# Optimization experiments

Hardware: AMD Instinct MI355X
Metric: run time of the kernel (lower is better)

## Reference

```python
import jax, jax.numpy as jnp
import numpy as np

EPS = 1e-8       # epsilon added to abs-diff in compute_sim
LN_EPS = 1e-5    # torch nn.LayerNorm default eps
NUM_HEADS = 8


def _layernorm(x, g, b):
    mu = jnp.mean(x, axis=-1, keepdims=True)
    var = jnp.mean((x - mu) ** 2, axis=-1, keepdims=True)
    return (x - mu) / jnp.sqrt(var + LN_EPS) * g + b


def _fla(x, alphas, betas):
    # x: [B, D]; alphas/betas: [H, 3] scalars per (head, {query,key,value})
    D = x.shape[-1]
    scale = 1.0 / jnp.sqrt(jnp.float32(D))
    acc = jnp.zeros_like(x)
    for h in range(alphas.shape[0]):  # small fixed head count; avoids H*B*D*D blowup
        q = alphas[h, 0] * x + betas[h, 0]
        k = alphas[h, 1] * x + betas[h, 1]
        v = alphas[h, 2] * x + betas[h, 2]
        # sim[b,i,j] = 1/(|q[b,j]-k[b,i]|+eps), softmax over j, scaled by 1/sqrt(D)
        sim = jax.nn.softmax(1.0 / (jnp.abs(q[:, None, :] - k[:, :, None]) + EPS), axis=-1) * scale
        acc = acc + jnp.einsum('bij,bj->bi', sim, v)
    return x + acc


def setup_inputs() -> dict:
    key = jax.random.key(0)
    ks = jax.random.split(key, 8)
    B, D, L = 1024, 256, 2  # batch, feature dim (input_dim == hidden dims), num hidden layers
    x = jax.random.normal(ks[0], (B, D), dtype=jnp.float32)
    fla_alphas = jax.random.uniform(ks[1], (L, NUM_HEADS, 3), dtype=jnp.float32)
    fla_betas = jax.random.uniform(ks[2], (L, NUM_HEADS, 3), dtype=jnp.float32)
    lim = 1.0 / np.sqrt(D)
    lin_W = jax.random.uniform(ks[3], (L, D, D), dtype=jnp.float32, minval=-lim, maxval=lim)
    lin_b = jax.random.uniform(ks[4], (L, D), dtype=jnp.float32, minval=-lim, maxval=lim)
    fla_ln_g = jnp.ones((L, D), jnp.float32)
    fla_ln_b = jnp.zeros((L, D), jnp.float32)
    lin_ln_g = jnp.ones((L, D), jnp.float32)
    lin_ln_b = jnp.zeros((L, D), jnp.float32)
    out_W = jax.random.uniform(ks[5], (D, 1), dtype=jnp.float32, minval=-lim, maxval=lim)
    out_b = jax.random.uniform(ks[6], (1,), dtype=jnp.float32, minval=-lim, maxval=lim)
    return dict(x=x, fla_alphas=fla_alphas, fla_betas=fla_betas,
                fla_ln_g=fla_ln_g, fla_ln_b=fla_ln_b,
                lin_W=lin_W, lin_b=lin_b,
                lin_ln_g=lin_ln_g, lin_ln_b=lin_ln_b,
                out_W=out_W, out_b=out_b)


def reference(x, fla_alphas, fla_betas, fla_ln_g, fla_ln_b,
              lin_W, lin_b, lin_ln_g, lin_ln_b, out_W, out_b):
    L = fla_alphas.shape[0]
    for i in range(L):
        x = _fla(x, fla_alphas[i], fla_betas[i])
        x = jax.nn.relu(x)
        x = _layernorm(x, fla_ln_g[i], fla_ln_b[i])
        x = x @ lin_W[i] + lin_b[i]
        x = jax.nn.relu(x)
        x = _layernorm(x, lin_ln_g[i], lin_ln_b[i])
    return x @ out_W + out_b
```

## Files before the change

### kernel.cpp

```cpp
#include <hip/hip_runtime.h>

#define DD 256
#define NH 8
#define HPT 2
#define NHG 4

constexpr float LN_EPS = 1e-5f;
constexpr float SCALE  = 0.0625f;
constexpr float KS     = 8.2629579e-8f;
constexpr float B_EXP  = 1064986816.0f;
constexpr float T0     = 1.36150e8f;
#define RCP_MAGIC 0x7EF311C3u

__device__ __forceinline__ float wexp_clamped(float dh, float Bh) {
    float y = __uint_as_float(RCP_MAGIC - __float_as_uint(dh));
    float w = fmaf(-fabsf(dh), fabsf(y), 2.0f);
    float f = fminf(fmaf(fabsf(y), w, Bh), B_EXP);
    unsigned u;
    asm("v_cvt_u32_f32 %0, %1" : "=v"(u) : "v"(f));
    return __uint_as_float(u);
}

__device__ __forceinline__ int lb256(const float* __restrict__ a, float t) {
    int p = 0;
    #pragma unroll
    for (int st = 128; st > 0; st >>= 1)
        p += (a[p + st - 1] < t) ? st : 0;
    return p;
}

__device__ __forceinline__ unsigned f2s(float f) {
    unsigned u = __float_as_uint(f);
    return (u & 0x80000000u) ? ~u : (u | 0x80000000u);
}
__device__ __forceinline__ float s2f(unsigned s) {
    unsigned u = (s & 0x80000000u) ? (s ^ 0x80000000u) : ~s;
    return __uint_as_float(u);
}

__device__ __forceinline__ float2 fla_head(const float* __restrict__ xsrt,
                                           float aqk, float ck) {
    float inv_aqk = __builtin_amdgcn_rcpf(aqk);
    float xstar = fminf(fmaxf(-ck * inv_aqk, -1e5f), 1e5f);
    int pos = lb256(xsrt, xstar);
    pos += (xsrt[pos] < xstar) ? 1 : 0;
    int i1 = (pos - 1 > 0) ? pos - 1 : 0;
    int i2 = (pos < DD - 1) ? pos : DD - 1;
    float x2 = xsrt[i2];
    float d1 = fabsf(fmaf(aqk, xsrt[i1], ck));
    float d2 = fabsf(fmaf(aqk, x2, ck));
    float dm = fminf(d1, d2);
    float ym = __uint_as_float(RCP_MAGIC - __float_as_uint(dm));
    float m  = fabsf(ym) * fmaf(-dm, fabsf(ym), 2.0f);
    float Bh = B_EXP - m;
    float mm = fmaf(m, 0.9375f, -T0);
    float halfw = (mm > 0.f) ? __builtin_amdgcn_rcpf(mm) * fabsf(inv_aqk)
                             : 3e38f;
    float vlo = xstar - halfw;
    float vhi = fmaxf(xstar + halfw, x2);
    int lo = lb256(xsrt, vlo); lo = (lo < i1) ? lo : i1;
    int hi = lb256(xsrt, vhi); hi += (xsrt[hi] < vhi) ? 1 : 0;
    hi = (hi > i2 + 1) ? hi : i2 + 1;

    const float4* xs4 = reinterpret_cast<const float4*>(xsrt);
    const int cLo = lo >> 2, cHi = (hi - 1) >> 2;
    float sE0=0.f,sE1=0.f,sE2=0.f,sE3=0.f;
    float sW0=0.f,sW1=0.f,sW2=0.f,sW3=0.f;
    #pragma unroll 2
    for (int ci = cLo; ci <= cHi; ++ci) {
        float4 xj = xs4[ci];
        float e0 = wexp_clamped(fmaf(aqk, xj.x, ck), Bh);
        float e1 = wexp_clamped(fmaf(aqk, xj.y, ck), Bh);
        float e2 = wexp_clamped(fmaf(aqk, xj.z, ck), Bh);
        float e3 = wexp_clamped(fmaf(aqk, xj.w, ck), Bh);
        sE0 += e0; sW0 = fmaf(e0, xj.x, sW0);
        sE1 += e1; sW1 = fmaf(e1, xj.y, sW1);
        sE2 += e2; sW2 = fmaf(e2, xj.z, sW2);
        sE3 += e3; sW3 = fmaf(e3, xj.w, sW3);
    }
    return make_float2((sE0+sE1)+(sE2+sE3), (sW0+sW1)+(sW2+sW3));
}

__device__ __forceinline__ float2 block_reduce2(float a, float b, float* sc, int tid) {
    #pragma unroll
    for (int off = 32; off; off >>= 1) {
        a += __shfl_down(a, off, 64);
        b += __shfl_down(b, off, 64);
    }
    __syncthreads();
    if ((tid & 63) == 0) { int w = tid >> 6; sc[w] = a; sc[16 + w] = b; }
    __syncthreads();
    const float4* s4 = reinterpret_cast<const float4*>(sc);
    float4 a0 = s4[0], a1 = s4[1], a2 = s4[2], a3 = s4[3];
    float4 b0 = s4[4], b1 = s4[5], b2 = s4[6], b3 = s4[7];
    float ra = ((a0.x+a0.y)+(a0.z+a0.w)) + ((a1.x+a1.y)+(a1.z+a1.w))
             + ((a2.x+a2.y)+(a2.z+a2.w)) + ((a3.x+a3.y)+(a3.z+a3.w));
    float rb = ((b0.x+b0.y)+(b0.z+b0.w)) + ((b1.x+b1.y)+(b1.z+b1.w))
             + ((b2.x+b2.y)+(b2.z+b2.w)) + ((b3.x+b3.y)+(b3.z+b3.w));
    return make_float2(ra, rb);
}

template<int LAST>
__global__ __launch_bounds__(1024, 8) void flann_layer(
    const float* __restrict__ x_in,
    const float* __restrict__ alphas,
    const float* __restrict__ betas,
    const float* __restrict__ g1, const float* __restrict__ b1,
    const float* __restrict__ W,  const float* __restrict__ wb,
    const float* __restrict__ g2, const float* __restrict__ b2,
    const float* __restrict__ outW, const float* __restrict__ outB,
    float* __restrict__ out)
{
    __shared__ __align__(16) float xsrt[DD];
    __shared__ __align__(16) float xln[DD];
    __shared__ float comb[NHG][DD];
    __shared__ float sc[32];
    __shared__ unsigned long long sflat[1024];

    const int tid  = threadIdx.x;
    const int i    = tid & (DD - 1);
    const int hg   = tid >> 8;
    const int bidx = blockIdx.x;

    const float* xrow = x_in + bidx * DD;
    float xv = xrow[i];

    float xr_v;  int idx_r;
    {
        unsigned long long v =
            ((unsigned long long)f2s(xv) << 8) | (unsigned)i;
        #pragma unroll
        for (int k = 2; k <= DD; k <<= 1) {
            #pragma unroll
            for (int j = k >> 1; j > 0; j >>= 1) {
                unsigned long long p;
                if (j < 64) {
                    p = __shfl_xor(v, j, 64);
                } else {
                    sflat[tid] = v;
                    __syncthreads();
                    p = sflat[tid ^ j];
                    __syncthreads();
                }
                bool keepmin = (((i & j) == 0) == ((i & k) == 0));
                v = keepmin ? (v < p ? v : p) : (v > p ? v : p);
            }
        }
        xr_v  = s2f((unsigned)(v >> 8));
        idx_r = (int)(v & 0xffu);
        if (hg == 0) xsrt[i] = xr_v;
        __syncthreads();
    }

    const int h0 = hg * HPT;
    const float aq0 = alphas[h0*3+0], ak0 = alphas[h0*3+1], av0 = alphas[h0*3+2];
    const float bq0 = betas [h0*3+0], bk0 = betas [h0*3+1], bv0 = betas [h0*3+2];
    const float aq1 = alphas[h0*3+3], ak1 = alphas[h0*3+4], av1 = alphas[h0*3+5];
    const float bq1 = betas [h0*3+3], bk1 = betas [h0*3+4], bv1 = betas [h0*3+5];
    const float aqk0 = aq0 * KS, aqk1 = aq1 * KS;
    const float ck0  = (bq0 - fmaf(ak0, xr_v, bk0)) * KS;
    const float ck1  = (bq1 - fmaf(ak1, xr_v, bk1)) * KS;

    float2 s0 = fla_head(xsrt, aqk0, ck0);
    float2 s1 = fla_head(xsrt, aqk1, ck1);

    float yE0 = __uint_as_float(RCP_MAGIC - __float_as_uint(s0.x));
    float rE0 = fabsf(yE0) * fmaf(-s0.x, fabsf(yE0), 2.0f);
    rE0 = rE0 * fmaf(-s0.x, rE0, 2.0f);
    float yE1 = __uint_as_float(RCP_MAGIC - __float_as_uint(s1.x));
    float rE1 = fabsf(yE1) * fmaf(-s1.x, fabsf(yE1), 2.0f);
    rE1 = rE1 * fmaf(-s1.x, rE1, 2.0f);
    float accp = fmaf(av0, s0.y, bv0 * s0.x) * rE0
               + fmaf(av1, s1.y, bv1 * s1.x) * rE1;
    comb[hg][idx_r] = accp;
    __syncthreads();

    float xr = 0.f;
    if (hg == 0) {
        float acc = (comb[0][i] + comb[1][i]) + (comb[2][i] + comb[3][i]);
        xr = fmaxf(fmaf(SCALE, acc, xv), 0.f);
    }

    float2 r = block_reduce2(xr, xr * xr, sc, tid);
    float mu  = r.x * (1.f / DD);
    float var = r.y * (1.f / DD) - mu * mu;
    if (hg == 0) {
        float xn = (xr - mu) * __builtin_amdgcn_rsqf(var + LN_EPS);
        xln[i] = fmaf(xn, g1[i], b1[i]);
    }
    __syncthreads();

    const float4* xl4 = reinterpret_cast<const float4*>(xln);
    float ga0 = (hg == 0) ? wb[i] : 0.f, ga1 = 0.f, ga2 = 0.f, ga3 = 0.f;
    #pragma unroll 4
    for (int d4 = 0; d4 < DD/16; ++d4) {
        int g4 = hg * (DD/16) + d4;
        float4 xd = xl4[g4];
        int dr = 4 * g4;
        ga0 = fmaf(xd.x, W[(dr + 0) * DD + i], ga0);
        ga1 = fmaf(xd.y, W[(dr + 1) * DD + i], ga1);
        ga2 = fmaf(xd.z, W[(dr + 2) * DD + i], ga2);
        ga3 = fmaf(xd.w, W[(dr + 3) * DD + i], ga3);
    }
    comb[hg][i] = (ga0 + ga1) + (ga2 + ga3);
    __syncthreads();

    float gv = 0.f;
    if (hg == 0)
        gv = fmaxf((comb[0][i] + comb[1][i]) + (comb[2][i] + comb[3][i]), 0.f);

    r = block_reduce2(gv, gv * gv, sc, tid);
    mu  = r.x * (1.f / DD);
    var = r.y * (1.f / DD) - mu * mu;
    float xo = 0.f;
    if (hg == 0)
        xo = fmaf((gv - mu) * __builtin_amdgcn_rsqf(var + LN_EPS), g2[i], b2[i]);

    if (!LAST) {
        if (hg == 0) out[bidx * DD + i] = xo;
    } else {
        float pr = (hg == 0) ? xo * outW[i] : 0.f;
        float2 p = block_reduce2(pr, 0.f, sc, tid);
        if (tid == 0) out[bidx] = p.x + outB[0];
    }
}

extern "C" void kernel_launch(void* const* d_in, const int* in_sizes, int n_in,
                              void* d_out, int out_size, void* d_ws, size_t ws_size,
                              hipStream_t stream) {
    const float* x      = (const float*)d_in[0];
    const float* alphas = (const float*)d_in[1];
    const float* betas  = (const float*)d_in[2];
    const float* flag   = (const float*)d_in[3];
    const float* flab   = (const float*)d_in[4];
    const float* linW   = (const float*)d_in[5];
    const float* linb   = (const float*)d_in[6];
    const float* ling   = (const float*)d_in[7];
    const float* linb2  = (const float*)d_in[8];
    const float* outW   = (const float*)d_in[9];
    const float* outB   = (const float*)d_in[10];

    const int B = in_sizes[0] / DD;
    float* ws   = (float*)d_ws;
    float* outp = (float*)d_out;

    dim3 grid(B), block(1024);
    flann_layer<0><<<grid, block, 0, stream>>>(
        x, alphas, betas, flag, flab, linW, linb, ling, linb2,
        nullptr, nullptr, ws);
    flann_layer<1><<<grid, block, 0, stream>>>(
        ws, alphas + NH*3, betas + NH*3, flag + DD, flab + DD,
        linW + DD*DD, linb + DD, ling + DD, linb2 + DD,
        outW, outB, outp);
}
```

Before: 158.0 us.

## Sort 32-bit keys, reuse LDS for sort scratch, interleave rows for wave balance

The bitonic sort now packs a truncated 24-bit sortable key plus the 8-bit index into 32 bits instead of 64. This halves the shuffle and LDS traffic and lets the sort scratch alias the comb buffer, dropping an 8KB shared array. The exact sorted values are recovered through an xorig lookup. Each thread now processes rows in an interleaved order (small and large sorted ranks alternate), which should balance the variable-length window scans within a wavefront. The bounds searches for both heads are hoisted ahead of the scans, and an extra barrier is added before comb is rewritten because it is now shared with the sort scratch.

```diff
diff --git a/kernel.cpp b/kernel.cpp
--- a/kernel.cpp
+++ b/kernel.cpp
@@ -33,13 +33,11 @@
     unsigned u = __float_as_uint(f);
     return (u & 0x80000000u) ? ~u : (u | 0x80000000u);
 }
-__device__ __forceinline__ float s2f(unsigned s) {
-    unsigned u = (s & 0x80000000u) ? (s ^ 0x80000000u) : ~s;
-    return __uint_as_float(u);
-}
-
-__device__ __forceinline__ float2 fla_head(const float* __restrict__ xsrt,
-                                           float aqk, float ck) {
+
+struct HeadCtx { float Bh; int cLo, cHi; };
+
+__device__ __forceinline__ HeadCtx fla_bounds(const float* __restrict__ xsrt,
+                                              float aqk, float ck) {
     float inv_aqk = __builtin_amdgcn_rcpf(aqk);
     float xstar = fminf(fmaxf(-ck * inv_aqk, -1e5f), 1e5f);
     int pos = lb256(xsrt, xstar);
@@ -52,7 +50,6 @@
     float dm = fminf(d1, d2);
     float ym = __uint_as_float(RCP_MAGIC - __float_as_uint(dm));
     float m  = fabsf(ym) * fmaf(-dm, fabsf(ym), 2.0f);
-    float Bh = B_EXP - m;
     float mm = fmaf(m, 0.9375f, -T0);
     float halfw = (mm > 0.f) ? __builtin_amdgcn_rcpf(mm) * fabsf(inv_aqk)
                              : 3e38f;
@@ -61,18 +58,22 @@
     int lo = lb256(xsrt, vlo); lo = (lo < i1) ? lo : i1;
     int hi = lb256(xsrt, vhi); hi += (xsrt[hi] < vhi) ? 1 : 0;
     hi = (hi > i2 + 1) ? hi : i2 + 1;
-
+    HeadCtx h; h.Bh = B_EXP - m; h.cLo = lo >> 2; h.cHi = (hi - 1) >> 2;
+    return h;
+}
+
+__device__ __forceinline__ float2 fla_scan(const float* __restrict__ xsrt,
+                                           float aqk, float ck, HeadCtx hc) {
     const float4* xs4 = reinterpret_cast<const float4*>(xsrt);
-    const int cLo = lo >> 2, cHi = (hi - 1) >> 2;
     float sE0=0.f,sE1=0.f,sE2=0.f,sE3=0.f;
     float sW0=0.f,sW1=0.f,sW2=0.f,sW3=0.f;
     #pragma unroll 2
-    for (int ci = cLo; ci <= cHi; ++ci) {
+    for (int ci = hc.cLo; ci <= hc.cHi; ++ci) {
         float4 xj = xs4[ci];
-        float e0 = wexp_clamped(fmaf(aqk, xj.x, ck), Bh);
-        float e1 = wexp_clamped(fmaf(aqk, xj.y, ck), Bh);
-        float e2 = wexp_clamped(fmaf(aqk, xj.z, ck), Bh);
-        float e3 = wexp_clamped(fmaf(aqk, xj.w, ck), Bh);
+        float e0 = wexp_clamped(fmaf(aqk, xj.x, ck), hc.Bh);
+        float e1 = wexp_clamped(fmaf(aqk, xj.y, ck), hc.Bh);
+        float e2 = wexp_clamped(fmaf(aqk, xj.z, ck), hc.Bh);
+        float e3 = wexp_clamped(fmaf(aqk, xj.w, ck), hc.Bh);
         sE0 += e0; sW0 = fmaf(e0, xj.x, sW0);
         sE1 += e1; sW1 = fmaf(e1, xj.y, sW1);
         sE2 += e2; sW2 = fmaf(e2, xj.z, sW2);
@@ -111,11 +112,12 @@
     const float* __restrict__ outW, const float* __restrict__ outB,
     float* __restrict__ out)
 {
+    __shared__ __align__(16) float xorig[DD];
     __shared__ __align__(16) float xsrt[DD];
     __shared__ __align__(16) float xln[DD];
+    __shared__ unsigned karr[DD];
     __shared__ float comb[NHG][DD];
     __shared__ float sc[32];
-    __shared__ unsigned long long sflat[1024];
 
     const int tid  = threadIdx.x;
     const int i    = tid & (DD - 1);
@@ -124,33 +126,39 @@
 
     const float* xrow = x_in + bidx * DD;
     float xv = xrow[i];
-
-    float xr_v;  int idx_r;
+    if (hg == 0) xorig[i] = xv;
+
     {
-        unsigned long long v =
-            ((unsigned long long)f2s(xv) << 8) | (unsigned)i;
+        unsigned v = (f2s(xv) & 0xFFFFFF00u) | (unsigned)i;
+        unsigned* flat = reinterpret_cast<unsigned*>(&comb[0][0]);
         #pragma unroll
         for (int k = 2; k <= DD; k <<= 1) {
             #pragma unroll
             for (int j = k >> 1; j > 0; j >>= 1) {
-                unsigned long long p;
+                unsigned p;
                 if (j < 64) {
-                    p = __shfl_xor(v, j, 64);
+                    p = (unsigned)__shfl_xor((int)v, j, 64);
                 } else {
-                    sflat[tid] = v;
+                    flat[tid] = v;
                     __syncthreads();
-                    p = sflat[tid ^ j];
+                    p = flat[tid ^ j];
                     __syncthreads();
                 }
                 bool keepmin = (((i & j) == 0) == ((i & k) == 0));
                 v = keepmin ? (v < p ? v : p) : (v > p ? v : p);
             }
         }
-        xr_v  = s2f((unsigned)(v >> 8));
-        idx_r = (int)(v & 0xffu);
-        if (hg == 0) xsrt[i] = xr_v;
+        if (hg == 0) {
+            karr[i] = v;
+            xsrt[i] = xorig[v & 0xFFu];
+        }
         __syncthreads();
     }
+
+    const int r     = (i & 1) ? (DD - 1) - (i >> 1) : (i >> 1);
+    const unsigned kr = karr[r];
+    const int idx_r = (int)(kr & 0xFFu);
+    const float xr_v = xsrt[r];
 
     const int h0 = hg * HPT;
     const float aq0 = alphas[h0*3+0], ak0 = alphas[h0*3+1], av0 = alphas[h0*3+2];
@@ -161,8 +169,10 @@
     const float ck0  = (bq0 - fmaf(ak0, xr_v, bk0)) * KS;
     const float ck1  = (bq1 - fmaf(ak1, xr_v, bk1)) * KS;
 
-    float2 s0 = fla_head(xsrt, aqk0, ck0);
-    float2 s1 = fla_head(xsrt, aqk1, ck1);
+    HeadCtx hc0 = fla_bounds(xsrt, aqk0, ck0);
+    HeadCtx hc1 = fla_bounds(xsrt, aqk1, ck1);
+    float2 s0 = fla_scan(xsrt, aqk0, ck0, hc0);
+    float2 s1 = fla_scan(xsrt, aqk1, ck1, hc1);
 
     float yE0 = __uint_as_float(RCP_MAGIC - __float_as_uint(s0.x));
     float rE0 = fabsf(yE0) * fmaf(-s0.x, fabsf(yE0), 2.0f);
@@ -172,6 +182,7 @@
     rE1 = rE1 * fmaf(-s1.x, rE1, 2.0f);
     float accp = fmaf(av0, s0.y, bv0 * s0.x) * rE0
                + fmaf(av1, s1.y, bv1 * s1.x) * rE1;
+    __syncthreads();
     comb[hg][idx_r] = accp;
     __syncthreads();
 
@@ -181,9 +192,9 @@
         xr = fmaxf(fmaf(SCALE, acc, xv), 0.f);
     }
 
-    float2 r = block_reduce2(xr, xr * xr, sc, tid);
-    float mu  = r.x * (1.f / DD);
-    float var = r.y * (1.f / DD) - mu * mu;
+    float2 rr = block_reduce2(xr, xr * xr, sc, tid);
+    float mu  = rr.x * (1.f / DD);
+    float var = rr.y * (1.f / DD) - mu * mu;
     if (hg == 0) {
         float xn = (xr - mu) * __builtin_amdgcn_rsqf(var + LN_EPS);
         xln[i] = fmaf(xn, g1[i], b1[i]);
@@ -209,9 +220,9 @@
     if (hg == 0)
         gv = fmaxf((comb[0][i] + comb[1][i]) + (comb[2][i] + comb[3][i]), 0.f);
 
-    r = block_reduce2(gv, gv * gv, sc, tid);
-    mu  = r.x * (1.f / DD);
-    var = r.y * (1.f / DD) - mu * mu;
+    rr = block_reduce2(gv, gv * gv, sc, tid);
+    mu  = rr.x * (1.f / DD);
+    var = rr.y * (1.f / DD) - mu * mu;
     float xo = 0.f;
     if (hg == 0)
         xo = fmaf((gv - mu) * __builtin_amdgcn_rsqf(var + LN_EPS), g2[i], b2[i]);
```

Result: no change. 155.5 us (-1.6%).
